# Kernel optimization log

Measured on AMD Instinct MI355X. Metric: run time of the kernel, lower is better.

The kernel has to match this reference:

```python
import jax, jax.numpy as jnp
import numpy as np

N_NODES = 100000
N_EDGES = 3200000
IN_F, HID, OUT = 3, 32, 1
NEG_SLOPE = 0.2


def _glorot(key, shape):
    fan_in, fan_out = shape[0], shape[-1]
    lim = jnp.sqrt(6.0 / (fan_in + fan_out)).astype(jnp.float32)
    return jax.random.uniform(key, shape, jnp.float32, -lim, lim)


def setup_inputs() -> dict:
    key = jax.random.key(0)
    ks = jax.random.split(key, 12)
    x = jax.random.normal(ks[0], (N_NODES, IN_F), jnp.float32)
    edge_index = jax.random.randint(ks[1], (2, N_EDGES), 0, N_NODES, jnp.int32)
    return {
        "x": x,
        "edge_index": edge_index,
        "W1": _glorot(ks[2], (IN_F, HID)),
        "att_src1": _glorot(ks[3], (1, HID))[0],
        "att_dst1": _glorot(ks[4], (1, HID))[0],
        "b1": jnp.zeros((HID,), jnp.float32),
        "W2": _glorot(ks[5], (HID, HID)),
        "att_src2": _glorot(ks[6], (1, HID))[0],
        "att_dst2": _glorot(ks[7], (1, HID))[0],
        "b2": jnp.zeros((HID,), jnp.float32),
        "Wl": _glorot(ks[8], (HID, OUT)),
        "bl": jnp.zeros((OUT,), jnp.float32),
    }


def gat_layer(x, src, dst, W, att_src, att_dst, b):
    # h: [N, HID] dense transform
    h = x @ W
    # per-node attention halves (compute once per node, gather per edge)
    a_s = h @ att_src  # [N]
    a_d = h @ att_dst  # [N]
    logits = jax.nn.leaky_relu(a_s[src] + a_d[dst], NEG_SLOPE)  # [E+N]
    # segment-softmax over incoming edges of each dst node
    m = jax.ops.segment_max(logits, dst, num_segments=N_NODES)
    m = jnp.where(jnp.isfinite(m), m, 0.0)
    ex = jnp.exp(logits - m[dst])
    denom = jax.ops.segment_sum(ex, dst, num_segments=N_NODES)
    coef = ex / (denom[dst] + 1e-16)
    # weighted scatter-aggregate of source messages
    out = jax.ops.segment_sum(coef[:, None] * h[src], dst, num_segments=N_NODES)
    return out + b


def reference(x, edge_index, W1, att_src1, att_dst1, b1, W2, att_src2, att_dst2, b2, Wl, bl):
    # PyG GATConv default: add self-loops
    loops = jnp.arange(N_NODES, dtype=edge_index.dtype)
    src = jnp.concatenate([edge_index[0], loops])
    dst = jnp.concatenate([edge_index[1], loops])
    h = gat_layer(x, src, dst, W1, att_src1, att_dst1, b1)
    h = jax.nn.relu(h)  # dropout is identity in eval
    h = gat_layer(h, src, dst, W2, att_src2, att_dst2, b2)
    h = jax.nn.relu(h)
    return h @ Wl + bl
```

## Files before the change

kernel.cpp:

```cpp
#include <hip/hip_runtime.h>
#include <hip/hip_fp16.h>

#define HID 32
#define BN 131
#define NBPAD 768
#define BSTRIDE 4608
#define CHUNK 4096
#define SPT_B 9
#define SPT_S 18

__device__ __forceinline__ float lrelu(float x) { return x > 0.0f ? x : 0.2f * x; }


__global__ void k_transform1(const float* __restrict__ x,
                             const float* __restrict__ W1,
                             const float* __restrict__ att_src,
                             const float* __restrict__ att_dst,
                             __half* __restrict__ hh,
                             float* __restrict__ a_s,
                             float* __restrict__ a_d,
                             int* __restrict__ cursor, int N)
{
    int tid = blockIdx.x * blockDim.x + threadIdx.x;
    if (tid < NBPAD) cursor[tid] = 0;
    int n = tid >> 5, f = tid & 31;
    if (n >= N) return;
    float x0 = x[n * 3 + 0], x1 = x[n * 3 + 1], x2 = x[n * 3 + 2];
    float hv = x0 * W1[f] + x1 * W1[HID + f] + x2 * W1[2 * HID + f];
    hh[(size_t)n * HID + f] = __float2half(hv);
    float as = hv * att_src[f];
    float ad = hv * att_dst[f];
    #pragma unroll
    for (int m = 16; m >= 1; m >>= 1) {
        as += __shfl_xor(as, m, 32);
        ad += __shfl_xor(ad, m, 32);
    }
    if (f == 0) { a_s[n] = as; a_d[n] = ad; }
}


struct BinSM {
    int stage[CHUNK];
    unsigned short sbid[CHUNK];
    int lhist[NBPAD], lexcl[NBPAD], lbase[NBPAD], lcur[NBPAD];
    int arr[256];
};

__global__ void __launch_bounds__(512) k_binscatter(const int* __restrict__ src,
        const int* __restrict__ dst, int* __restrict__ cursor,
        unsigned int* __restrict__ packed, int NBr, int E)
{
    __shared__ BinSM S;
    const int BLK = 512;
    int t = threadIdx.x;
    int base = blockIdx.x * CHUNK;
    for (int i = t; i < NBPAD; i += BLK) { S.lhist[i] = 0; S.lcur[i] = 0; }
    __syncthreads();
    int cnt = E - base; if (cnt > CHUNK) cnt = CHUNK;
    for (int i = t; i < cnt; i += BLK)
        atomicAdd(&S.lhist[dst[base + i] / BN], 1);
    __syncthreads();
    int b0 = 3 * t;
    int c0 = 0, c1 = 0, c2 = 0, s = 0;
    if (t < 256) {
        c0 = S.lhist[b0]; c1 = S.lhist[b0 + 1]; c2 = S.lhist[b0 + 2];
        s = c0 + c1 + c2;
        S.arr[t] = s;
    }
    __syncthreads();
    for (int o = 1; o < 256; o <<= 1) {
        int v = (t < 256 && t >= o) ? S.arr[t - o] : 0;
        __syncthreads();
        if (t < 256) S.arr[t] += v;
        __syncthreads();
    }
    if (t < 256) {
        int ex = S.arr[t] - s;
        int e0 = ex, e1 = ex + c0, e2 = ex + c0 + c1;
        S.lexcl[b0] = e0; S.lexcl[b0 + 1] = e1; S.lexcl[b0 + 2] = e2;
        for (int i = 0; i < c0; ++i) S.sbid[e0 + i] = (unsigned short)b0;
        for (int i = 0; i < c1; ++i) S.sbid[e1 + i] = (unsigned short)(b0 + 1);
        for (int i = 0; i < c2; ++i) S.sbid[e2 + i] = (unsigned short)(b0 + 2);
    }
    for (int b = t; b < NBr; b += BLK)
        if (S.lhist[b]) S.lbase[b] = b * BSTRIDE + atomicAdd(&cursor[b], S.lhist[b]);
    __syncthreads();
    for (int i = t; i < cnt; i += BLK) {
        int d = dst[base + i];
        int sv = src[base + i];
        int b = d / BN;
        int dl = d - b * BN;
        int idx = S.lexcl[b] + atomicAdd(&S.lcur[b], 1);
        S.stage[idx] = (int)((unsigned)sv | ((unsigned)dl << 17));
    }
    __syncthreads();
    for (int i = t; i < cnt; i += BLK) {
        int b = S.sbid[i];
        int gpos = S.lbase[b] + (i - S.lexcl[b]);
        if (gpos < (b + 1) * BSTRIDE)
            packed[gpos] = (unsigned)S.stage[i];
    }
}


__global__ void __launch_bounds__(256) k_sort(const int* __restrict__ cursor,
        unsigned int* __restrict__ packed, int* __restrict__ nmeta, int N)
{
    __shared__ int hist[256];
    __shared__ int scn[256];
    __shared__ int stage[BSTRIDE];

    int bk = blockIdx.x, t = threadIdx.x;
    int cnt = cursor[bk]; if (cnt > BSTRIDE) cnt = BSTRIDE;
    hist[t] = 0;
    __syncthreads();

    unsigned pk[SPT_S];
    #pragma unroll
    for (int u = 0; u < SPT_S; ++u) {
        int i = t + u * 256;
        if (i < cnt) {
            pk[u] = packed[(size_t)bk * BSTRIDE + i];
            atomicAdd(&hist[(pk[u] >> 17) & 255], 1);
        }
    }
    __syncthreads();

    scn[t] = hist[t];
    __syncthreads();
    for (int o = 1; o < 256; o <<= 1) {
        int v = (t >= o) ? scn[t - o] : 0;
        __syncthreads();
        scn[t] += v;
        __syncthreads();
    }
    int cdeg = hist[t];
    int ex = scn[t] - cdeg;
    hist[t] = ex;
    if (t < BN) {
        int n = bk * BN + t;
        if (n < N) nmeta[n] = ex | (cdeg << 16);
    }
    __syncthreads();

    #pragma unroll
    for (int u = 0; u < SPT_S; ++u) {
        int i = t + u * 256;
        if (i < cnt) {
            int idx = atomicAdd(&hist[(pk[u] >> 17) & 255], 1);
            stage[idx] = (int)pk[u];
        }
    }
    __syncthreads();

    for (int i = t; i < cnt; i += 256)
        packed[(size_t)bk * BSTRIDE + i] = (unsigned)stage[i];
}


struct AggSM {
    int2  lpair[BSTRIDE];
    float adT[BN];
    float asT[BN];
    int   meta[BN];
};

__device__ __forceinline__ void build_stream(AggSM& S,
        const unsigned int* __restrict__ pk, int cnt,
        const float* __restrict__ a_s, const float* __restrict__ a_d,
        const int* __restrict__ nmeta, int nodeBase, int N)
{
    int t = threadIdx.x;
    if (t < BN) {
        int n = nodeBase + t;
        bool ok = n < N;
        S.meta[t] = ok ? nmeta[n] : 0;
        S.adT[t]  = ok ? a_d[n] : 0.0f;
        S.asT[t]  = ok ? a_s[n] : 0.0f;
    }
    __syncthreads();
    #pragma unroll
    for (int u = 0; u < SPT_B; ++u) {
        int i = t + u * 512;
        if (i < cnt) {
            unsigned p = pk[i];
            int sv = (int)(p & 0x1FFFF);
            int dl = (p >> 17) & 255;
            float e = __expf(lrelu(a_s[sv] + S.adT[dl]));
            S.lpair[i] = make_int2(sv, __float_as_int(e));
        }
    }
    __syncthreads();
}

__device__ __forceinline__ void agg_node8(const __half* __restrict__ hh,
        float exs, const float* __restrict__ b, int n, int f,
        const int2* lpair, int off, int dg,
        float& v0, float& v1, float& v2, float& v3)
{
    uint2 us = *(const uint2*)(hh + (size_t)n * HID + 4 * f);
    float2 s01 = __half22float2(*(__half2*)&us.x);
    float2 s23 = __half22float2(*(__half2*)&us.y);
    float den = exs;
    float a0 = exs * s01.x, a1 = exs * s01.y, a2 = exs * s23.x, a3 = exs * s23.y;

    int j = 0;
    for (; j + 8 <= dg; j += 8) {
        int2 p[8]; uint2 uu[8];
        #pragma unroll
        for (int q = 0; q < 8; ++q) p[q] = lpair[off + j + q];
        #pragma unroll
        for (int q = 0; q < 8; ++q)
            uu[q] = *(const uint2*)(hh + (size_t)p[q].x * HID + 4 * f);
        #pragma unroll
        for (int q = 0; q < 8; ++q) {
            float e = __int_as_float(p[q].y);
            float2 qa = __half22float2(*(__half2*)&uu[q].x);
            float2 qb = __half22float2(*(__half2*)&uu[q].y);
            den += e;
            a0 = fmaf(e, qa.x, a0); a1 = fmaf(e, qa.y, a1);
            a2 = fmaf(e, qb.x, a2); a3 = fmaf(e, qb.y, a3);
        }
    }
    for (; j < dg; ++j) {
        int2 pp = lpair[off + j];
        uint2 uu = *(const uint2*)(hh + (size_t)pp.x * HID + 4 * f);
        float e = __int_as_float(pp.y);
        float2 qa = __half22float2(*(__half2*)&uu.x);
        float2 qb = __half22float2(*(__half2*)&uu.y);
        den += e;
        a0 = fmaf(e, qa.x, a0); a1 = fmaf(e, qa.y, a1);
        a2 = fmaf(e, qb.x, a2); a3 = fmaf(e, qb.y, a3);
    }
    float inv = 1.0f / (den + 1e-16f);
    float4 bb = *(const float4*)(b + 4 * f);
    v0 = fmaxf(a0 * inv + bb.x, 0.0f);
    v1 = fmaxf(a1 * inv + bb.y, 0.0f);
    v2 = fmaxf(a2 * inv + bb.z, 0.0f);
    v3 = fmaxf(a3 * inv + bb.w, 0.0f);
}

__device__ __forceinline__ void epi_mid8(int n, int f,
        float v0, float v1, float v2, float v3,
        const float* __restrict__ W2, const float* __restrict__ as2w,
        const float* __restrict__ ad2w,
        __half* __restrict__ hh_out, float* __restrict__ as_out,
        float* __restrict__ ad_out)
{
    float h0 = 0.0f, h1 = 0.0f, h2 = 0.0f, h3 = 0.0f;
    #pragma unroll
    for (int k = 0; k < 8; ++k) {
        float aa[4];
        aa[0] = __shfl(v0, k, 8);
        aa[1] = __shfl(v1, k, 8);
        aa[2] = __shfl(v2, k, 8);
        aa[3] = __shfl(v3, k, 8);
        const float* wr = W2 + (4 * k) * HID + 4 * f;
        #pragma unroll
        for (int c = 0; c < 4; ++c) {
            float4 w = *(const float4*)(wr + c * HID);
            h0 = fmaf(aa[c], w.x, h0);
            h1 = fmaf(aa[c], w.y, h1);
            h2 = fmaf(aa[c], w.z, h2);
            h3 = fmaf(aa[c], w.w, h3);
        }
    }
    __half2 o01 = __floats2half2_rn(h0, h1);
    __half2 o23 = __floats2half2_rn(h2, h3);
    uint2 st;
    st.x = *(unsigned*)&o01;
    st.y = *(unsigned*)&o23;
    *(uint2*)(hh_out + (size_t)n * HID + 4 * f) = st;

    float4 asw = *(const float4*)(as2w + 4 * f);
    float4 adw = *(const float4*)(ad2w + 4 * f);
    float as = h0 * asw.x + h1 * asw.y + h2 * asw.z + h3 * asw.w;
    float ad = h0 * adw.x + h1 * adw.y + h2 * adw.z + h3 * adw.w;
    #pragma unroll
    for (int m2 = 4; m2 >= 1; m2 >>= 1) {
        as += __shfl_xor(as, m2, 8);
        ad += __shfl_xor(ad, m2, 8);
    }
    if (f == 0) { as_out[n] = as; ad_out[n] = ad; }
}


__global__ void __launch_bounds__(512) k_agg_mid(const __half* __restrict__ hh,
        const float* __restrict__ a_s, const float* __restrict__ a_d,
        const int* __restrict__ cursor, const unsigned int* __restrict__ packed,
        const int* __restrict__ nmeta,
        const float* __restrict__ b1, const float* __restrict__ W2,
        const float* __restrict__ as2w, const float* __restrict__ ad2w,
        __half* __restrict__ hh_out, float* __restrict__ as_out,
        float* __restrict__ ad_out, int N)
{
    __shared__ AggSM S;
    int bk = blockIdx.x, t = threadIdx.x;
    int cnt = cursor[bk]; if (cnt > BSTRIDE) cnt = BSTRIDE;
    build_stream(S, packed + (size_t)bk * BSTRIDE, cnt, a_s, a_d,
                 nmeta, bk * BN, N);
    int g = t >> 3, f = t & 7;
    for (int dl = g; dl < BN; dl += 64) {
        int n = bk * BN + dl;
        if (n >= N) continue;
        int m = S.meta[dl];
        int off = m & 0xFFFF, dg = m >> 16;
        float exs = __expf(lrelu(S.asT[dl] + S.adT[dl]));
        float v0, v1, v2, v3;
        agg_node8(hh, exs, b1, n, f, S.lpair, off, dg, v0, v1, v2, v3);
        epi_mid8(n, f, v0, v1, v2, v3, W2, as2w, ad2w, hh_out, as_out, ad_out);
    }
}

__global__ void __launch_bounds__(512) k_agg_out(const __half* __restrict__ hh,
        const float* __restrict__ a_s, const float* __restrict__ a_d,
        const int* __restrict__ cursor, const unsigned int* __restrict__ packed,
        const int* __restrict__ nmeta,
        const float* __restrict__ b2, const float* __restrict__ Wl,
        const float* __restrict__ bl, float* __restrict__ out, int N)
{
    __shared__ AggSM S;
    int bk = blockIdx.x, t = threadIdx.x;
    int cnt = cursor[bk]; if (cnt > BSTRIDE) cnt = BSTRIDE;
    build_stream(S, packed + (size_t)bk * BSTRIDE, cnt, a_s, a_d,
                 nmeta, bk * BN, N);
    int g = t >> 3, f = t & 7;
    for (int dl = g; dl < BN; dl += 64) {
        int n = bk * BN + dl;
        if (n >= N) continue;
        int m = S.meta[dl];
        int off = m & 0xFFFF, dg = m >> 16;
        float exs = __expf(lrelu(S.asT[dl] + S.adT[dl]));
        float v0, v1, v2, v3;
        agg_node8(hh, exs, b2, n, f, S.lpair, off, dg, v0, v1, v2, v3);
        float4 wl = *(const float4*)(Wl + 4 * f);
        float y = v0 * wl.x + v1 * wl.y + v2 * wl.z + v3 * wl.w;
        #pragma unroll
        for (int m2 = 4; m2 >= 1; m2 >>= 1)
            y += __shfl_xor(y, m2, 8);
        if (f == 0) out[n] = y + bl[0];
    }
}


extern "C" void kernel_launch(void* const* d_in, const int* in_sizes, int n_in,
                              void* d_out, int out_size, void* d_ws, size_t ws_size,
                              hipStream_t stream)
{
    const float* x        = (const float*)d_in[0];
    const int*   eidx     = (const int*)d_in[1];
    const float* W1       = (const float*)d_in[2];
    const float* att_src1 = (const float*)d_in[3];
    const float* att_dst1 = (const float*)d_in[4];
    const float* b1       = (const float*)d_in[5];
    const float* W2       = (const float*)d_in[6];
    const float* att_src2 = (const float*)d_in[7];
    const float* att_dst2 = (const float*)d_in[8];
    const float* b2       = (const float*)d_in[9];
    const float* Wl       = (const float*)d_in[10];
    const float* bl       = (const float*)d_in[11];
    float* out = (float*)d_out;

    int N = in_sizes[0] / 3;
    int E = in_sizes[1] / 2;
    const int* src = eidx;
    const int* dst = eidx + E;
    int NBr = (N + BN - 1) / BN;

    size_t szNHh = (size_t)N * HID * 2;
    size_t szN4  = (size_t)N * 4;
    size_t szPK  = (size_t)NBr * BSTRIDE * 4;

    char* ws = (char*)d_ws;
    __half* h1h    = (__half*)ws; ws += szNHh;
    __half* h2h    = (__half*)ws; ws += szNHh;
    unsigned int* packed = (unsigned int*)ws; ws += szPK;
    float*  a_s1   = (float*)ws;  ws += szN4;
    float*  a_d1   = (float*)ws;  ws += szN4;
    float*  a_s2   = (float*)ws;  ws += szN4;
    float*  a_d2   = (float*)ws;  ws += szN4;
    int*    nmeta  = (int*)ws;    ws += szN4;
    int*    cursor = (int*)ws;    ws += NBPAD * 4;

    const int B = 256;
    int gridNode32 = (N * HID + B - 1) / B;
    int gridBin    = (E + CHUNK - 1) / CHUNK;

    k_transform1<<<gridNode32, B, 0, stream>>>(x, W1, att_src1, att_dst1,
                                               h1h, a_s1, a_d1, cursor, N);
    k_binscatter<<<gridBin, 512, 0, stream>>>(src, dst, cursor, packed, NBr, E);
    k_sort<<<NBr, 256, 0, stream>>>(cursor, packed, nmeta, N);
    k_agg_mid<<<NBr, 512, 0, stream>>>(h1h, a_s1, a_d1, cursor, packed, nmeta,
                                       b1, W2, att_src2, att_dst2,
                                       h2h, a_s2, a_d2, N);
    k_agg_out<<<NBr, 512, 0, stream>>>(h2h, a_s2, a_d2, cursor, packed, nmeta,
                                       b2, Wl, bl, out, N);
}
```

Baseline: 260.5 us.

## Fold per-bucket sort into aggregation kernels and split node edges across two octets

Removes the separate k_sort kernel and instead builds a per-bucket CSR in shared memory inside each aggregation kernel, using a histogram, a scan and an atomic scatter. Binscatter now holds its edges in registers with larger chunks so src/dst are read once, and the global bucket cursors are padded to avoid contention. Aggregation hands out nodes through a shared-memory work queue, with two 8-lane groups per node that each take half the edges and then combine with shuffles. The CSR build is now repeated in both aggregation kernels, and the shared atomic queue adds overhead.

```diff
diff --git a/kernel.cpp b/kernel.cpp
--- a/kernel.cpp
+++ b/kernel.cpp
@@ -5,9 +5,9 @@
 #define BN 131
 #define NBPAD 768
 #define BSTRIDE 4608
-#define CHUNK 4096
-#define SPT_B 9
-#define SPT_S 18
+#define CHUNK 6144
+#define EPT 12
+#define CPAD 16
 
 __device__ __forceinline__ float lrelu(float x) { return x > 0.0f ? x : 0.2f * x; }
 
@@ -22,7 +22,7 @@
                              int* __restrict__ cursor, int N)
 {
     int tid = blockIdx.x * blockDim.x + threadIdx.x;
-    if (tid < NBPAD) cursor[tid] = 0;
+    if (tid < NBPAD * CPAD) cursor[tid] = 0;
     int n = tid >> 5, f = tid & 31;
     if (n >= N) return;
     float x0 = x[n * 3 + 0], x1 = x[n * 3 + 1], x2 = x[n * 3 + 2];
@@ -51,15 +51,25 @@
         unsigned int* __restrict__ packed, int NBr, int E)
 {
     __shared__ BinSM S;
-    const int BLK = 512;
     int t = threadIdx.x;
     int base = blockIdx.x * CHUNK;
-    for (int i = t; i < NBPAD; i += BLK) { S.lhist[i] = 0; S.lcur[i] = 0; }
-    __syncthreads();
     int cnt = E - base; if (cnt > CHUNK) cnt = CHUNK;
-    for (int i = t; i < cnt; i += BLK)
-        atomicAdd(&S.lhist[dst[base + i] / BN], 1);
-    __syncthreads();
+
+    for (int i = t; i < NBPAD; i += 512) { S.lhist[i] = 0; S.lcur[i] = 0; }
+    __syncthreads();
+
+    int myd[EPT], mys[EPT];
+    #pragma unroll
+    for (int u = 0; u < EPT; ++u) {
+        int i = t + u * 512;
+        myd[u] = -1;
+        if (i < cnt) { myd[u] = dst[base + i]; mys[u] = src[base + i]; }
+    }
+    #pragma unroll
+    for (int u = 0; u < EPT; ++u)
+        if (myd[u] >= 0) atomicAdd(&S.lhist[myd[u] / BN], 1);
+    __syncthreads();
+
     int b0 = 3 * t;
     int c0 = 0, c1 = 0, c2 = 0, s = 0;
     if (t < 256) {
@@ -82,19 +92,24 @@
         for (int i = 0; i < c1; ++i) S.sbid[e1 + i] = (unsigned short)(b0 + 1);
         for (int i = 0; i < c2; ++i) S.sbid[e2 + i] = (unsigned short)(b0 + 2);
     }
-    for (int b = t; b < NBr; b += BLK)
-        if (S.lhist[b]) S.lbase[b] = b * BSTRIDE + atomicAdd(&cursor[b], S.lhist[b]);
-    __syncthreads();
-    for (int i = t; i < cnt; i += BLK) {
-        int d = dst[base + i];
-        int sv = src[base + i];
-        int b = d / BN;
-        int dl = d - b * BN;
-        int idx = S.lexcl[b] + atomicAdd(&S.lcur[b], 1);
-        S.stage[idx] = (int)((unsigned)sv | ((unsigned)dl << 17));
-    }
-    __syncthreads();
-    for (int i = t; i < cnt; i += BLK) {
+    for (int b = t; b < NBr; b += 512)
+        if (S.lhist[b])
+            S.lbase[b] = b * BSTRIDE + atomicAdd(&cursor[b * CPAD], S.lhist[b]);
+    __syncthreads();
+
+    #pragma unroll
+    for (int u = 0; u < EPT; ++u) {
+        if (myd[u] >= 0) {
+            int d = myd[u];
+            int b = d / BN;
+            int dl = d - b * BN;
+            int idx = S.lexcl[b] + atomicAdd(&S.lcur[b], 1);
+            S.stage[idx] = (int)((unsigned)mys[u] | ((unsigned)dl << 17));
+        }
+    }
+    __syncthreads();
+
+    for (int i = t; i < cnt; i += 512) {
         int b = S.sbid[i];
         int gpos = S.lbase[b] + (i - S.lexcl[b]);
         if (gpos < (b + 1) * BSTRIDE)
@@ -103,112 +118,62 @@
 }
 
 
-__global__ void __launch_bounds__(256) k_sort(const int* __restrict__ cursor,
-        unsigned int* __restrict__ packed, int* __restrict__ nmeta, int N)
-{
-    __shared__ int hist[256];
-    __shared__ int scn[256];
-    __shared__ int stage[BSTRIDE];
-
-    int bk = blockIdx.x, t = threadIdx.x;
-    int cnt = cursor[bk]; if (cnt > BSTRIDE) cnt = BSTRIDE;
-    hist[t] = 0;
-    __syncthreads();
-
-    unsigned pk[SPT_S];
-    #pragma unroll
-    for (int u = 0; u < SPT_S; ++u) {
-        int i = t + u * 256;
-        if (i < cnt) {
-            pk[u] = packed[(size_t)bk * BSTRIDE + i];
-            atomicAdd(&hist[(pk[u] >> 17) & 255], 1);
-        }
-    }
-    __syncthreads();
-
-    scn[t] = hist[t];
-    __syncthreads();
-    for (int o = 1; o < 256; o <<= 1) {
-        int v = (t >= o) ? scn[t - o] : 0;
-        __syncthreads();
-        scn[t] += v;
-        __syncthreads();
-    }
-    int cdeg = hist[t];
-    int ex = scn[t] - cdeg;
-    hist[t] = ex;
-    if (t < BN) {
-        int n = bk * BN + t;
-        if (n < N) nmeta[n] = ex | (cdeg << 16);
-    }
-    __syncthreads();
-
-    #pragma unroll
-    for (int u = 0; u < SPT_S; ++u) {
-        int i = t + u * 256;
-        if (i < cnt) {
-            int idx = atomicAdd(&hist[(pk[u] >> 17) & 255], 1);
-            stage[idx] = (int)pk[u];
-        }
-    }
-    __syncthreads();
-
-    for (int i = t; i < cnt; i += 256)
-        packed[(size_t)bk * BSTRIDE + i] = (unsigned)stage[i];
-}
-
-
 struct AggSM {
     int2  lpair[BSTRIDE];
+    int   lhist[256], lscan[256], lcur[256];
     float adT[BN];
-    float asT[BN];
-    int   meta[BN];
+    int   qnext;
 };
 
-__device__ __forceinline__ void build_stream(AggSM& S,
+__device__ __forceinline__ void build_csr(AggSM& S,
         const unsigned int* __restrict__ pk, int cnt,
         const float* __restrict__ a_s, const float* __restrict__ a_d,
-        const int* __restrict__ nmeta, int nodeBase, int N)
+        int nodeBase, int N)
 {
     int t = threadIdx.x;
-    if (t < BN) {
-        int n = nodeBase + t;
-        bool ok = n < N;
-        S.meta[t] = ok ? nmeta[n] : 0;
-        S.adT[t]  = ok ? a_d[n] : 0.0f;
-        S.asT[t]  = ok ? a_s[n] : 0.0f;
-    }
-    __syncthreads();
-    #pragma unroll
-    for (int u = 0; u < SPT_B; ++u) {
-        int i = t + u * 512;
-        if (i < cnt) {
-            unsigned p = pk[i];
-            int sv = (int)(p & 0x1FFFF);
-            int dl = (p >> 17) & 255;
-            float e = __expf(lrelu(a_s[sv] + S.adT[dl]));
-            S.lpair[i] = make_int2(sv, __float_as_int(e));
-        }
-    }
-    __syncthreads();
-}
-
-__device__ __forceinline__ void agg_node8(const __half* __restrict__ hh,
-        float exs, const float* __restrict__ b, int n, int f,
+    if (t < 256) { S.lhist[t] = 0; S.lcur[t] = 0; }
+    if (t < BN) { int n = nodeBase + t; S.adT[t] = (n < N) ? a_d[n] : 0.0f; }
+    if (t == 0) S.qnext = 0;
+    __syncthreads();
+    for (int i = t; i < cnt; i += 512)
+        atomicAdd(&S.lhist[(pk[i] >> 17) & 255], 1);
+    __syncthreads();
+    if (t < 256) S.lscan[t] = S.lhist[t];
+    __syncthreads();
+    for (int o = 1; o < 256; o <<= 1) {
+        int v = (t < 256 && t >= o) ? S.lscan[t - o] : 0;
+        __syncthreads();
+        if (t < 256) S.lscan[t] += v;
+        __syncthreads();
+    }
+    for (int i = t; i < cnt; i += 512) {
+        unsigned p = pk[i];
+        int dl = (p >> 17) & 255;
+        int sv = (int)(p & 0x1FFFF);
+        float e = __expf(lrelu(a_s[sv] + S.adT[dl]));
+        int pos = atomicAdd(&S.lcur[dl], 1);
+        S.lpair[(S.lscan[dl] - S.lhist[dl]) + pos] = make_int2(sv, __float_as_int(e));
+    }
+    __syncthreads();
+}
+
+__device__ __forceinline__ void agg_node2w(const __half* __restrict__ hh,
+        float exs, int n, int f, int oct,
         const int2* lpair, int off, int dg,
-        float& v0, float& v1, float& v2, float& v3)
+        float& v0, float& v1, float& v2, float& v3, float& deno)
 {
     uint2 us = *(const uint2*)(hh + (size_t)n * HID + 4 * f);
     float2 s01 = __half22float2(*(__half2*)&us.x);
     float2 s23 = __half22float2(*(__half2*)&us.y);
-    float den = exs;
-    float a0 = exs * s01.x, a1 = exs * s01.y, a2 = exs * s23.x, a3 = exs * s23.y;
+    float m = (oct == 0) ? exs : 0.0f;
+    float den = m;
+    float a0 = m * s01.x, a1 = m * s01.y, a2 = m * s23.x, a3 = m * s23.y;
 
     int j = 0;
-    for (; j + 8 <= dg; j += 8) {
+    for (; j + 16 <= dg; j += 16) {
         int2 p[8]; uint2 uu[8];
         #pragma unroll
-        for (int q = 0; q < 8; ++q) p[q] = lpair[off + j + q];
+        for (int q = 0; q < 8; ++q) p[q] = lpair[off + j + 2 * q + oct];
         #pragma unroll
         for (int q = 0; q < 8; ++q)
             uu[q] = *(const uint2*)(hh + (size_t)p[q].x * HID + 4 * f);
@@ -222,25 +187,39 @@
             a2 = fmaf(e, qb.x, a2); a3 = fmaf(e, qb.y, a3);
         }
     }
-    for (; j < dg; ++j) {
-        int2 pp = lpair[off + j];
+    for (; j < dg; j += 2) {
+        int idx = j + oct;
+        int cl = idx < dg ? idx : dg - 1;
+        int2 pp = lpair[off + cl];
+        float e = (idx < dg) ? __int_as_float(pp.y) : 0.0f;
         uint2 uu = *(const uint2*)(hh + (size_t)pp.x * HID + 4 * f);
-        float e = __int_as_float(pp.y);
         float2 qa = __half22float2(*(__half2*)&uu.x);
         float2 qb = __half22float2(*(__half2*)&uu.y);
         den += e;
         a0 = fmaf(e, qa.x, a0); a1 = fmaf(e, qa.y, a1);
         a2 = fmaf(e, qb.x, a2); a3 = fmaf(e, qb.y, a3);
     }
+    den += __shfl_xor(den, 8, 16);
+    a0 += __shfl_xor(a0, 8, 16);
+    a1 += __shfl_xor(a1, 8, 16);
+    a2 += __shfl_xor(a2, 8, 16);
+    a3 += __shfl_xor(a3, 8, 16);
+    deno = den;
+    v0 = a0; v1 = a1; v2 = a2; v3 = a3;
+}
+
+__device__ __forceinline__ void finish_relu(float den, const float* __restrict__ b,
+        int f, float& v0, float& v1, float& v2, float& v3)
+{
     float inv = 1.0f / (den + 1e-16f);
     float4 bb = *(const float4*)(b + 4 * f);
-    v0 = fmaxf(a0 * inv + bb.x, 0.0f);
-    v1 = fmaxf(a1 * inv + bb.y, 0.0f);
-    v2 = fmaxf(a2 * inv + bb.z, 0.0f);
-    v3 = fmaxf(a3 * inv + bb.w, 0.0f);
-}
-
-__device__ __forceinline__ void epi_mid8(int n, int f,
+    v0 = fmaxf(v0 * inv + bb.x, 0.0f);
+    v1 = fmaxf(v1 * inv + bb.y, 0.0f);
+    v2 = fmaxf(v2 * inv + bb.z, 0.0f);
+    v3 = fmaxf(v3 * inv + bb.w, 0.0f);
+}
+
+__device__ __forceinline__ void epi_mid8(int n, int f, int oct,
         float v0, float v1, float v2, float v3,
         const float* __restrict__ W2, const float* __restrict__ as2w,
         const float* __restrict__ ad2w,
@@ -265,13 +244,14 @@
             h3 = fmaf(aa[c], w.w, h3);
         }
     }
-    __half2 o01 = __floats2half2_rn(h0, h1);
-    __half2 o23 = __floats2half2_rn(h2, h3);
-    uint2 st;
-    st.x = *(unsigned*)&o01;
-    st.y = *(unsigned*)&o23;
-    *(uint2*)(hh_out + (size_t)n * HID + 4 * f) = st;
-
+    if (oct == 0) {
+        __half2 o01 = __floats2half2_rn(h0, h1);
+        __half2 o23 = __floats2half2_rn(h2, h3);
+        uint2 st;
+        st.x = *(unsigned*)&o01;
+        st.y = *(unsigned*)&o23;
+        *(uint2*)(hh_out + (size_t)n * HID + 4 * f) = st;
+    }
     float4 asw = *(const float4*)(as2w + 4 * f);
     float4 adw = *(const float4*)(ad2w + 4 * f);
     float as = h0 * asw.x + h1 * asw.y + h2 * asw.z + h3 * asw.w;
@@ -281,14 +261,13 @@
         as += __shfl_xor(as, m2, 8);
         ad += __shfl_xor(ad, m2, 8);
     }
-    if (f == 0) { as_out[n] = as; ad_out[n] = ad; }
+    if (f == 0 && oct == 0) { as_out[n] = as; ad_out[n] = ad; }
 }
 
 
 __global__ void __launch_bounds__(512) k_agg_mid(const __half* __restrict__ hh,
         const float* __restrict__ a_s, const float* __restrict__ a_d,
         const int* __restrict__ cursor, const unsigned int* __restrict__ packed,
-        const int* __restrict__ nmeta,
         const float* __restrict__ b1, const float* __restrict__ W2,
         const float* __restrict__ as2w, const float* __restrict__ ad2w,
         __half* __restrict__ hh_out, float* __restrict__ as_out,
@@ -296,49 +275,56 @@
 {
     __shared__ AggSM S;
     int bk = blockIdx.x, t = threadIdx.x;
-    int cnt = cursor[bk]; if (cnt > BSTRIDE) cnt = BSTRIDE;
-    build_stream(S, packed + (size_t)bk * BSTRIDE, cnt, a_s, a_d,
-                 nmeta, bk * BN, N);
-    int g = t >> 3, f = t & 7;
-    for (int dl = g; dl < BN; dl += 64) {
+    int cnt = cursor[bk * CPAD]; if (cnt > BSTRIDE) cnt = BSTRIDE;
+    build_csr(S, packed + (size_t)bk * BSTRIDE, cnt, a_s, a_d, bk * BN, N);
+    int lane = t & 15, f = lane & 7, oct = lane >> 3;
+    for (;;) {
+        int dl;
+        if (lane == 0) dl = atomicAdd(&S.qnext, 1);
+        dl = __shfl(dl, 0, 16);
+        if (dl >= BN) break;
         int n = bk * BN + dl;
         if (n >= N) continue;
-        int m = S.meta[dl];
-        int off = m & 0xFFFF, dg = m >> 16;
-        float exs = __expf(lrelu(S.asT[dl] + S.adT[dl]));
-        float v0, v1, v2, v3;
-        agg_node8(hh, exs, b1, n, f, S.lpair, off, dg, v0, v1, v2, v3);
-        epi_mid8(n, f, v0, v1, v2, v3, W2, as2w, ad2w, hh_out, as_out, ad_out);
+        int off = S.lscan[dl] - S.lhist[dl];
+        int dg = S.lhist[dl];
+        float exs = __expf(lrelu(a_s[n] + S.adT[dl]));
+        float v0, v1, v2, v3, den;
+        agg_node2w(hh, exs, n, f, oct, S.lpair, off, dg, v0, v1, v2, v3, den);
+        finish_relu(den, b1, f, v0, v1, v2, v3);
+        epi_mid8(n, f, oct, v0, v1, v2, v3, W2, as2w, ad2w, hh_out, as_out, ad_out);
     }
 }
 
 __global__ void __launch_bounds__(512) k_agg_out(const __half* __restrict__ hh,
         const float* __restrict__ a_s, const float* __restrict__ a_d,
         const int* __restrict__ cursor, const unsigned int* __restrict__ packed,
-        const int* __restrict__ nmeta,
         const float* __restrict__ b2, const float* __restrict__ Wl,
         const float* __restrict__ bl, float* __restrict__ out, int N)
 {
     __shared__ AggSM S;
     int bk = blockIdx.x, t = threadIdx.x;
-    int cnt = cursor[bk]; if (cnt > BSTRIDE) cnt = BSTRIDE;
-    build_stream(S, packed + (size_t)bk * BSTRIDE, cnt, a_s, a_d,
-                 nmeta, bk * BN, N);
-    int g = t >> 3, f = t & 7;
-    for (int dl = g; dl < BN; dl += 64) {
+    int cnt = cursor[bk * CPAD]; if (cnt > BSTRIDE) cnt = BSTRIDE;
+    build_csr(S, packed + (size_t)bk * BSTRIDE, cnt, a_s, a_d, bk * BN, N);
+    int lane = t & 15, f = lane & 7, oct = lane >> 3;
+    for (;;) {
+        int dl;
+        if (lane == 0) dl = atomicAdd(&S.qnext, 1);
+        dl = __shfl(dl, 0, 16);
+        if (dl >= BN) break;
         int n = bk * BN + dl;
         if (n >= N) continue;
-        int m = S.meta[dl];
-        int off = m & 0xFFFF, dg = m >> 16;
-        float exs = __expf(lrelu(S.asT[dl] + S.adT[dl]));
-        float v0, v1, v2, v3;
-        agg_node8(hh, exs, b2, n, f, S.lpair, off, dg, v0, v1, v2, v3);
+        int off = S.lscan[dl] - S.lhist[dl];
+        int dg = S.lhist[dl];
+        float exs = __expf(lrelu(a_s[n] + S.adT[dl]));
+        float v0, v1, v2, v3, den;
+        agg_node2w(hh, exs, n, f, oct, S.lpair, off, dg, v0, v1, v2, v3, den);
+        finish_relu(den, b2, f, v0, v1, v2, v3);
         float4 wl = *(const float4*)(Wl + 4 * f);
         float y = v0 * wl.x + v1 * wl.y + v2 * wl.z + v3 * wl.w;
         #pragma unroll
         for (int m2 = 4; m2 >= 1; m2 >>= 1)
             y += __shfl_xor(y, m2, 8);
-        if (f == 0) out[n] = y + bl[0];
+        if (lane == 0) out[n] = y + bl[0];
     }
 }
 
@@ -379,8 +365,7 @@
     float*  a_d1   = (float*)ws;  ws += szN4;
     float*  a_s2   = (float*)ws;  ws += szN4;
     float*  a_d2   = (float*)ws;  ws += szN4;
-    int*    nmeta  = (int*)ws;    ws += szN4;
-    int*    cursor = (int*)ws;    ws += NBPAD * 4;
+    int*    cursor = (int*)ws;    ws += (size_t)NBPAD * CPAD * 4;
 
     const int B = 256;
     int gridNode32 = (N * HID + B - 1) / B;
@@ -389,10 +374,9 @@
     k_transform1<<<gridNode32, B, 0, stream>>>(x, W1, att_src1, att_dst1,
                                                h1h, a_s1, a_d1, cursor, N);
     k_binscatter<<<gridBin, 512, 0, stream>>>(src, dst, cursor, packed, NBr, E);
-    k_sort<<<NBr, 256, 0, stream>>>(cursor, packed, nmeta, N);
-    k_agg_mid<<<NBr, 512, 0, stream>>>(h1h, a_s1, a_d1, cursor, packed, nmeta,
+    k_agg_mid<<<NBr, 512, 0, stream>>>(h1h, a_s1, a_d1, cursor, packed,
                                        b1, W2, att_src2, att_dst2,
                                        h2h, a_s2, a_d2, N);
-    k_agg_out<<<NBr, 512, 0, stream>>>(h2h, a_s2, a_d2, cursor, packed, nmeta,
+    k_agg_out<<<NBr, 512, 0, stream>>>(h2h, a_s2, a_d2, cursor, packed,
                                        b2, Wl, bl, out, N);
 }
```

Result: slower. 272.9 us (+4.8%).
